# Optimization experiments

Measured on AMD Instinct MI355X. Metric: run time of the kernel, lower is better.

The kernel has to match this reference:

```python
import jax, jax.numpy as jnp
import numpy as np

E = 256
H = 512
LN_EPS = 1e-5
NORM_EPS = 1e-12


def setup_inputs() -> dict:
    key = jax.random.key(0)
    ks = jax.random.split(key, 8)
    B, N, M = 8, 128, 128
    track_features = jax.random.normal(ks[0], (B, N, E), dtype=jnp.float32)
    det_features = jax.random.normal(ks[1], (B, M, E), dtype=jnp.float32)
    # MLP params (torch Linear default init style: uniform, but values irrelevant for correctness harness)
    lim1 = 1.0 / np.sqrt(3 * E)
    W1 = jax.random.uniform(ks[2], (3 * E, H), minval=-lim1, maxval=lim1, dtype=jnp.float32)
    b1 = jax.random.uniform(ks[3], (H,), minval=-lim1, maxval=lim1, dtype=jnp.float32)
    gamma = jnp.ones((H,), dtype=jnp.float32)
    beta = jnp.zeros((H,), dtype=jnp.float32)
    lim2 = 1.0 / np.sqrt(H)
    W2 = jax.random.uniform(ks[4], (H, 1), minval=-lim2, maxval=lim2, dtype=jnp.float32)
    b2 = jax.random.uniform(ks[5], (1,), minval=-lim2, maxval=lim2, dtype=jnp.float32)
    return {"track_features": track_features, "det_features": det_features,
            "W1": W1, "b1": b1, "gamma": gamma, "beta": beta, "W2": W2, "b2": b2}


def _l2_normalize(x):
    # F.normalize(x, dim=-1): x / max(||x||_2, eps)
    n = jnp.sqrt(jnp.sum(x * x, axis=-1, keepdims=True))
    return x / jnp.maximum(n, NORM_EPS)


def reference(track_features, det_features, W1, b1, gamma, beta, W2, b2):
    t = _l2_normalize(track_features)   # (B, N, E)
    d = _l2_normalize(det_features)     # (B, M, E)
    tb = t[:, :, None, :]               # (B, N, 1, E)
    db = d[:, None, :, :]               # (B, 1, M, E)
    B, N, _ = t.shape
    M = d.shape[1]
    diff = jnp.abs(tb - db)                                  # (B, N, M, E)
    pair = jnp.concatenate([jnp.broadcast_to(tb, (B, N, M, E)),
                            jnp.broadcast_to(db, (B, N, M, E)),
                            diff], axis=-1)                  # (B, N, M, 3E)
    h = jnp.einsum('bnme,eh->bnmh', pair, W1) + b1           # (B, N, M, H)
    mu = jnp.mean(h, axis=-1, keepdims=True)
    var = jnp.mean((h - mu) ** 2, axis=-1, keepdims=True)
    h = (h - mu) * jax.lax.rsqrt(var + LN_EPS) * gamma + beta
    h = h * jax.nn.sigmoid(h)                                # SiLU
    out = jnp.einsum('bnmh,ho->bnmo', h, W2)[..., 0] + b2[0]  # (B, N, M)
    return out
```

## Files before the change

kernel.cpp:

```cpp
#include <hip/hip_runtime.h>
#include <hip/hip_bf16.h>
#include <cstdint>

typedef __bf16 bf16x8 __attribute__((ext_vector_type(8)));
typedef __bf16 bf16x2 __attribute__((ext_vector_type(2)));
typedef float f32x4 __attribute__((ext_vector_type(4)));
typedef float f32x2 __attribute__((ext_vector_type(2)));

#define E_DIM 256
#define H_DIM 512

static __device__ __forceinline__ unsigned pkbf(float a, float b) {
    bf16x2 h;
    h[0] = (__bf16)a;
    h[1] = (__bf16)b;
    return __builtin_bit_cast(unsigned, h);
}

__global__ __launch_bounds__(512, 2)
void prep_kernel(const float* __restrict__ track, const float* __restrict__ det,
                 const float* __restrict__ W1, const float* __restrict__ b1,
                 float* __restrict__ P, float* __restrict__ Q,
                 __bf16* __restrict__ W1cc, float* __restrict__ sclT,
                 float* __restrict__ sclD, float* __restrict__ out) {
    __shared__ __align__(16) __bf16 Ash[16 * 256];
    int tid  = threadIdx.x;
    int blk  = blockIdx.x;
    int lane = tid & 63;
    int wave = tid >> 6;
    int lq   = lane >> 4;
    int lc   = lane & 15;
    int l5   = lane & 31;

    int mat  = blk >> 8;
    int rowg = (blk >> 2) & 63;
    int hq   = blk & 3;
    int r0   = rowg * 16;
    int h0   = hq * 128;
    const float* src = mat ? det : track;

    if (tid < 32) {
        int u = blk * 32 + tid;
        int j = u & 3;
        int h = (u >> 2) & 511;
        int c = u >> 11;
        const float* s = W1 + (size_t)(512 + c * 32 + j * 8) * H_DIM + h;
        uint4 v;
        v.x = pkbf(s[0],                 s[(size_t)1 * H_DIM]);
        v.y = pkbf(s[(size_t)2 * H_DIM], s[(size_t)3 * H_DIM]);
        v.z = pkbf(s[(size_t)4 * H_DIM], s[(size_t)5 * H_DIM]);
        v.w = pkbf(s[(size_t)6 * H_DIM], s[(size_t)7 * H_DIM]);
        *(uint4*)(W1cc + ((size_t)(c * 512 + h) * 32 + j * 8)) = v;
    } else if (tid < 96) {
        float4 z = {0.f, 0.f, 0.f, 0.f};
        ((float4*)out)[blk * 64 + (tid - 32)] = z;
    }

    {
        int row = wave * 2 + (lane >> 5);
        const float* gp = src + (size_t)(r0 + row) * E_DIM + l5 * 8;
        float4 x0 = *(const float4*)gp;
        float4 x1 = *(const float4*)(gp + 4);
        float ss = x0.x*x0.x + x0.y*x0.y + x0.z*x0.z + x0.w*x0.w
                 + x1.x*x1.x + x1.y*x1.y + x1.z*x1.z + x1.w*x1.w;
#pragma unroll
        for (int off = 16; off > 0; off >>= 1) ss += __shfl_xor(ss, off);
        float st = 1.0f / fmaxf(sqrtf(ss), 1e-12f);
        if (hq == 0 && l5 == 0) (mat ? sclD : sclT)[r0 + row] = st;
        uint4 v;
        v.x = pkbf(x0.x * st, x0.y * st);
        v.y = pkbf(x0.z * st, x0.w * st);
        v.z = pkbf(x1.x * st, x1.y * st);
        v.w = pkbf(x1.z * st, x1.w * st);
        int cc = l5 >> 2, j = l5 & 3;
        *(uint4*)&Ash[(size_t)(cc * 64 + j * 16 + row) * 8] = v;
    }
    __syncthreads();

    int hB = h0 + wave * 16 + lc;
    const float* wb = W1 + (size_t)(mat * 256) * H_DIM + hB;
    float wf[8];
#pragma unroll
    for (int i = 0; i < 8; ++i)
        wf[i] = wb[(size_t)(lq * 8 + i) * H_DIM];

    f32x4 acc = (f32x4){0.f, 0.f, 0.f, 0.f};

#pragma unroll
    for (int c = 0; c < 8; ++c) {
        uint4 u;
        u.x = pkbf(wf[0], wf[1]);
        u.y = pkbf(wf[2], wf[3]);
        u.z = pkbf(wf[4], wf[5]);
        u.w = pkbf(wf[6], wf[7]);
        bf16x8 cw = __builtin_bit_cast(bf16x8, u);
        if (c < 7) {
            const float* nb = wb + (size_t)((c + 1) * 32 + lq * 8) * H_DIM;
#pragma unroll
            for (int i = 0; i < 8; ++i)
                wf[i] = nb[(size_t)i * H_DIM];
        }
        bf16x8 af = *(const bf16x8*)&Ash[(size_t)(c * 64 + lane) * 8];
        acc = __builtin_amdgcn_mfma_f32_16x16x32_bf16(cw, af, acc, 0, 0, 0);
    }

    float* dst = mat ? Q : P;
    int h = h0 + wave * 16 + lq * 4;
    f32x4 o = acc;
    if (!mat) o += *(const f32x4*)&b1[h];
    *(f32x4*)&dst[(size_t)(r0 + lc) * H_DIM + h] = o;
}

__global__ __launch_bounds__(512, 4)
void main_kernel(const float* __restrict__ track, const float* __restrict__ det,
                 const __bf16* __restrict__ W1cc,
                 const float* __restrict__ P, const float* __restrict__ Q,
                 const float* __restrict__ sclT, const float* __restrict__ sclD,
                 const float* __restrict__ gamma, const float* __restrict__ beta,
                 const float* __restrict__ W2, const float* __restrict__ b2,
                 float* __restrict__ out) {
    __shared__ __align__(16) char SMEM[44032];
    __bf16* Ash  = (__bf16*)SMEM;
    float*  LNr1 = (float*)(SMEM + 32768);
    float*  LNr2 = (float*)(SMEM + 35072);
    float*  AS   = (float*)(SMEM + 37376);
    float*  BS   = (float*)(SMEM + 37632);
    float*  Gs   = (float*)(SMEM + 37888);
    float*  Bs   = (float*)(SMEM + 39936);
    float*  Ws   = (float*)(SMEM + 41984);

    int tid  = threadIdx.x;
    int lane = tid & 63;
    int wave = tid >> 6;
    int lq   = lane >> 4;
    int lc   = lane & 15;

    int i   = blockIdx.x;
    int xcd = i & 7;
    int t8  = (i >> 3) & 31;
    int b   = i >> 8;
    int n0  = ((xcd >> 1) * 4 + (t8 >> 3)) * 8;
    int m0  = ((xcd & 1) * 8 + (t8 & 7)) * 8;
    int gn  = b * 128 + n0;
    int gm  = b * 128 + m0;

    float b2v = b2[0];
    Gs[tid] = gamma[tid];
    Bs[tid] = beta[tid];
    Ws[tid] = W2[tid];

    const uint4* Wg = (const uint4*)W1cc;
    int hb = wave * 64 + lc;
    bf16x8 bwA[4], bwB[4];
#pragma unroll
    for (int ht = 0; ht < 4; ++ht)
        bwA[ht] = __builtin_bit_cast(bf16x8, Wg[(hb + ht * 16) * 4 + lq]);

    int k0 = wave * 32 + lq * 8;
    int ml = lane & 7;
    float sd = sclD[gm + ml];
    const float* dr = det + (size_t)(gm + ml) * E_DIM + k0;
    float4 d0 = *(const float4*)dr;
    float4 d1 = *(const float4*)(dr + 4);
#pragma unroll
    for (int r = 0; r < 4; ++r) {
        int nl = r * 2 + (lc >> 3);
        float st = sclT[gn + nl];
        const float* tr = track + (size_t)(gn + nl) * E_DIM + k0;
        float4 t0 = *(const float4*)tr;
        float4 t1 = *(const float4*)(tr + 4);
        uint4 v;
        v.x = pkbf(fabsf(t0.x * st - d0.x * sd), fabsf(t0.y * st - d0.y * sd));
        v.y = pkbf(fabsf(t0.z * st - d0.z * sd), fabsf(t0.w * st - d0.w * sd));
        v.z = pkbf(fabsf(t1.x * st - d1.x * sd), fabsf(t1.y * st - d1.y * sd));
        v.w = pkbf(fabsf(t1.z * st - d1.z * sd), fabsf(t1.w * st - d1.w * sd));
        *(uint4*)&Ash[(size_t)(r * 512 + wave * 64 + lane) * 8] = v;
    }

    const float* Pb = P + (size_t)gn * H_DIM;
    const float* Qb = Q + (size_t)gm * H_DIM;
    f32x4 acc[4][4];
    {
        f32x4 qv[4];
#pragma unroll
        for (int ht = 0; ht < 4; ++ht)
            qv[ht] = *(const f32x4*)&Qb[(size_t)ml * H_DIM + wave * 64 + ht * 16 + lq * 4];
#pragma unroll
        for (int pt = 0; pt < 4; ++pt) {
            int n = pt * 2 + (lc >> 3);
#pragma unroll
            for (int ht = 0; ht < 4; ++ht) {
                f32x4 pv = *(const f32x4*)&Pb[(size_t)n * H_DIM + wave * 64 + ht * 16 + lq * 4];
                acc[pt][ht] = pv + qv[ht];
            }
        }
    }
    __syncthreads();

#pragma unroll 2
    for (int c = 0; c < 8; ++c) {
        bf16x8* cur = (c & 1) ? bwB : bwA;
        bf16x8* nxt = (c & 1) ? bwA : bwB;
        int c1 = (c + 1) & 7;
#pragma unroll
        for (int ht = 0; ht < 4; ++ht)
            nxt[ht] = __builtin_bit_cast(bf16x8, Wg[c1 * 2048 + (hb + ht * 16) * 4 + lq]);
        __builtin_amdgcn_s_setprio(1);
#pragma unroll
        for (int pt = 0; pt < 4; ++pt) {
            bf16x8 af = *(const bf16x8*)&Ash[(size_t)((pt * 8 + c) * 64 + lane) * 8];
#pragma unroll
            for (int ht = 0; ht < 4; ++ht)
                acc[pt][ht] = __builtin_amdgcn_mfma_f32_16x16x32_bf16(cur[ht], af, acc[pt][ht], 0, 0, 0);
        }
        __builtin_amdgcn_s_setprio(0);
    }

#pragma unroll
    for (int pt = 0; pt < 4; ++pt) {
        f32x2 s1v = (f32x2){0.f, 0.f}, s2v = (f32x2){0.f, 0.f};
#pragma unroll
        for (int ht = 0; ht < 4; ++ht) {
#pragma unroll
            for (int hf = 0; hf < 2; ++hf) {
                f32x2 v = (f32x2){acc[pt][ht][hf * 2], acc[pt][ht][hf * 2 + 1]};
                s1v += v;
                s2v += v * v;
            }
        }
        float s1 = s1v[0] + s1v[1];
        float s2 = s2v[0] + s2v[1];
        s1 += __shfl_xor(s1, 16); s2 += __shfl_xor(s2, 16);
        s1 += __shfl_xor(s1, 32); s2 += __shfl_xor(s2, 32);
        if (lq == 0) {
            LNr1[(pt * 16 + lc) * 9 + wave] = s1;
            LNr2[(pt * 16 + lc) * 9 + wave] = s2;
        }
    }
    __syncthreads();
    {
        int p = tid >> 3, w = tid & 7;
        float s1 = LNr1[p * 9 + w];
        float s2 = LNr2[p * 9 + w];
        s1 += __shfl_xor(s1, 1); s2 += __shfl_xor(s2, 1);
        s1 += __shfl_xor(s1, 2); s2 += __shfl_xor(s2, 2);
        s1 += __shfl_xor(s1, 4); s2 += __shfl_xor(s2, 4);
        if (w == 0) {
            float mu  = s1 * (1.0f / 512.0f);
            float var = s2 * (1.0f / 512.0f) - mu * mu;
            float rs  = rsqrtf(var + 1e-5f);
            AS[p] = rs;
            BS[p] = -mu * rs;
        }
    }
    __syncthreads();

    float as[4], bs[4];
#pragma unroll
    for (int pt = 0; pt < 4; ++pt) { as[pt] = AS[pt * 16 + lc]; bs[pt] = BS[pt * 16 + lc]; }
    f32x2 cav[4];
#pragma unroll
    for (int pt = 0; pt < 4; ++pt) cav[pt] = (f32x2){0.f, 0.f};
#pragma unroll
    for (int ht = 0; ht < 4; ++ht) {
        int h = wave * 64 + ht * 16 + lq * 4;
        f32x4 g  = *(const f32x4*)&Gs[h];
        f32x4 bb = *(const f32x4*)&Bs[h];
        f32x4 w  = *(const f32x4*)&Ws[h];
#pragma unroll
        for (int pt = 0; pt < 4; ++pt) {
            f32x2 a2  = (f32x2){as[pt], as[pt]};
            f32x2 b2p = (f32x2){bs[pt], bs[pt]};
#pragma unroll
            for (int hf = 0; hf < 2; ++hf) {
                f32x2 v  = (f32x2){acc[pt][ht][hf * 2], acc[pt][ht][hf * 2 + 1]};
                f32x2 gg = (f32x2){g[hf * 2],  g[hf * 2 + 1]};
                f32x2 bv = (f32x2){bb[hf * 2], bb[hf * 2 + 1]};
                f32x2 wv = (f32x2){w[hf * 2],  w[hf * 2 + 1]};
                f32x2 x  = (v * a2 + b2p) * gg + bv;
                f32x2 xw = x * wv;
                f32x2 e, sg;
                e[0]  = __expf(-x[0]);
                e[1]  = __expf(-x[1]);
                sg[0] = __builtin_amdgcn_rcpf(1.0f + e[0]);
                sg[1] = __builtin_amdgcn_rcpf(1.0f + e[1]);
                cav[pt] += xw * sg;
            }
        }
    }
#pragma unroll
    for (int pt = 0; pt < 4; ++pt) {
        float cg = cav[pt][0] + cav[pt][1];
        cg += __shfl_xor(cg, 16);
        cg += __shfl_xor(cg, 32);
        if (lq == 0) {
            if (wave == 0) cg += b2v;
            int n = pt * 2 + (lc >> 3);
            int m = lc & 7;
            atomicAdd(&out[(size_t)(gn + n) * 128 + m0 + m], cg);
        }
    }
}

extern "C" void kernel_launch(void* const* d_in, const int* in_sizes, int n_in,
                              void* d_out, int out_size, void* d_ws, size_t ws_size,
                              hipStream_t stream) {
    const float* track = (const float*)d_in[0];
    const float* det   = (const float*)d_in[1];
    const float* W1    = (const float*)d_in[2];
    const float* b1    = (const float*)d_in[3];
    const float* gamma = (const float*)d_in[4];
    const float* beta  = (const float*)d_in[5];
    const float* W2    = (const float*)d_in[6];
    const float* b2    = (const float*)d_in[7];
    float* out = (float*)d_out;

    char* ws = (char*)d_ws;
    float*  Pp   = (float*)(ws);
    float*  Qp   = (float*)(ws + (2u << 20));
    __bf16* W1cc = (__bf16*)(ws + (4u << 20));
    float*  sclT = (float*)(ws + (4u << 20) + (256u << 10));
    float*  sclD = (float*)(ws + (4u << 20) + (264u << 10));

    prep_kernel<<<512, 512, 0, stream>>>(track, det, W1, b1, Pp, Qp, W1cc, sclT, sclD, out);
    main_kernel<<<2048, 512, 0, stream>>>(track, det, W1cc, Pp, Qp, sclT, sclD,
                                          gamma, beta, W2, b2, out);
}
```

Baseline: 142.2 us.

## Process two detection tiles per block with overlapped next-tile staging

Each main_kernel block now handles two consecutive 8-row detection tiles for the same 8 track rows, halving the grid to 1024 blocks. The second tile's pair-difference staging into shared memory is issued between the LayerNorm reduction barriers, and its P+Q accumulator init is issued after the first tile's atomics. The goal is to amortize per-block setup (gamma/beta/W2 staging, first W1 fragment loads) and overlap global loads with epilogue work. The cost is half as many blocks to fill the device and a longer serial chain within each block.

```diff
diff --git a/kernel.cpp b/kernel.cpp
--- a/kernel.cpp
+++ b/kernel.cpp
@@ -110,6 +110,47 @@
     if (!mat) o += *(const f32x4*)&b1[h];
     *(f32x4*)&dst[(size_t)(r0 + lc) * H_DIM + h] = o;
 }
+
+#define A_STAGE(GM)                                                                     \
+    {                                                                                   \
+        int k0 = wave * 32 + lq * 8;                                                    \
+        float sd = sclD[(GM) + ml];                                                     \
+        const float* drp = det + (size_t)((GM) + ml) * E_DIM + k0;                      \
+        float4 d0 = *(const float4*)drp;                                                \
+        float4 d1 = *(const float4*)(drp + 4);                                          \
+        _Pragma("unroll")                                                               \
+        for (int r = 0; r < 4; ++r) {                                                   \
+            int nl = r * 2 + (lc >> 3);                                                 \
+            float st = sclT[gn + nl];                                                   \
+            const float* trp = track + (size_t)(gn + nl) * E_DIM + k0;                  \
+            float4 t0 = *(const float4*)trp;                                            \
+            float4 t1 = *(const float4*)(trp + 4);                                      \
+            uint4 vv;                                                                   \
+            vv.x = pkbf(fabsf(t0.x * st - d0.x * sd), fabsf(t0.y * st - d0.y * sd));    \
+            vv.y = pkbf(fabsf(t0.z * st - d0.z * sd), fabsf(t0.w * st - d0.w * sd));    \
+            vv.z = pkbf(fabsf(t1.x * st - d1.x * sd), fabsf(t1.y * st - d1.y * sd));    \
+            vv.w = pkbf(fabsf(t1.z * st - d1.z * sd), fabsf(t1.w * st - d1.w * sd));    \
+            *(uint4*)&Ash[(size_t)(r * 512 + wave * 64 + lane) * 8] = vv;               \
+        }                                                                               \
+    }
+
+#define C_INIT(GM)                                                                      \
+    {                                                                                   \
+        const float* Qb = Q + (size_t)(GM) * H_DIM;                                     \
+        f32x4 qv[4];                                                                    \
+        _Pragma("unroll")                                                               \
+        for (int ht = 0; ht < 4; ++ht)                                                  \
+            qv[ht] = *(const f32x4*)&Qb[(size_t)ml * H_DIM + wave * 64 + ht * 16 + lq * 4]; \
+        _Pragma("unroll")                                                               \
+        for (int pt = 0; pt < 4; ++pt) {                                                \
+            int n = pt * 2 + (lc >> 3);                                                 \
+            _Pragma("unroll")                                                           \
+            for (int ht = 0; ht < 4; ++ht) {                                            \
+                f32x4 pv = *(const f32x4*)&Pb[(size_t)n * H_DIM + wave * 64 + ht * 16 + lq * 4]; \
+                acc[pt][ht] = pv + qv[ht];                                              \
+            }                                                                           \
+        }                                                                               \
+    }
 
 __global__ __launch_bounds__(512, 4)
 void main_kernel(const float* __restrict__ track, const float* __restrict__ det,
@@ -134,15 +175,16 @@
     int wave = tid >> 6;
     int lq   = lane >> 4;
     int lc   = lane & 15;
+    int ml   = lane & 7;
 
     int i   = blockIdx.x;
     int xcd = i & 7;
-    int t8  = (i >> 3) & 31;
-    int b   = i >> 8;
-    int n0  = ((xcd >> 1) * 4 + (t8 >> 3)) * 8;
-    int m0  = ((xcd & 1) * 8 + (t8 & 7)) * 8;
+    int t4  = (i >> 3) & 15;
+    int b   = i >> 7;
+    int n0  = ((xcd >> 1) * 4 + (t4 >> 2)) * 8;
+    int mp0 = ((xcd & 1) * 4 + (t4 & 3)) * 16;
     int gn  = b * 128 + n0;
-    int gm  = b * 128 + m0;
+    int gm0 = b * 128 + mp0;
 
     float b2v = b2[0];
     Gs[tid] = gamma[tid];
@@ -156,148 +198,123 @@
     for (int ht = 0; ht < 4; ++ht)
         bwA[ht] = __builtin_bit_cast(bf16x8, Wg[(hb + ht * 16) * 4 + lq]);
 
-    int k0 = wave * 32 + lq * 8;
-    int ml = lane & 7;
-    float sd = sclD[gm + ml];
-    const float* dr = det + (size_t)(gm + ml) * E_DIM + k0;
-    float4 d0 = *(const float4*)dr;
-    float4 d1 = *(const float4*)(dr + 4);
-#pragma unroll
-    for (int r = 0; r < 4; ++r) {
-        int nl = r * 2 + (lc >> 3);
-        float st = sclT[gn + nl];
-        const float* tr = track + (size_t)(gn + nl) * E_DIM + k0;
-        float4 t0 = *(const float4*)tr;
-        float4 t1 = *(const float4*)(tr + 4);
-        uint4 v;
-        v.x = pkbf(fabsf(t0.x * st - d0.x * sd), fabsf(t0.y * st - d0.y * sd));
-        v.y = pkbf(fabsf(t0.z * st - d0.z * sd), fabsf(t0.w * st - d0.w * sd));
-        v.z = pkbf(fabsf(t1.x * st - d1.x * sd), fabsf(t1.y * st - d1.y * sd));
-        v.w = pkbf(fabsf(t1.z * st - d1.z * sd), fabsf(t1.w * st - d1.w * sd));
-        *(uint4*)&Ash[(size_t)(r * 512 + wave * 64 + lane) * 8] = v;
-    }
-
     const float* Pb = P + (size_t)gn * H_DIM;
-    const float* Qb = Q + (size_t)gm * H_DIM;
     f32x4 acc[4][4];
-    {
-        f32x4 qv[4];
-#pragma unroll
-        for (int ht = 0; ht < 4; ++ht)
-            qv[ht] = *(const f32x4*)&Qb[(size_t)ml * H_DIM + wave * 64 + ht * 16 + lq * 4];
+
+    A_STAGE(gm0)
+    C_INIT(gm0)
+    __syncthreads();
+
+#pragma unroll 1
+    for (int j = 0; j < 2; ++j) {
+#pragma unroll 2
+        for (int c = 0; c < 8; ++c) {
+            bf16x8* cur = (c & 1) ? bwB : bwA;
+            bf16x8* nxt = (c & 1) ? bwA : bwB;
+            int c1 = (c + 1) & 7;
+#pragma unroll
+            for (int ht = 0; ht < 4; ++ht)
+                nxt[ht] = __builtin_bit_cast(bf16x8, Wg[c1 * 2048 + (hb + ht * 16) * 4 + lq]);
+            __builtin_amdgcn_s_setprio(1);
+#pragma unroll
+            for (int pt = 0; pt < 4; ++pt) {
+                bf16x8 af = *(const bf16x8*)&Ash[(size_t)((pt * 8 + c) * 64 + lane) * 8];
+#pragma unroll
+                for (int ht = 0; ht < 4; ++ht)
+                    acc[pt][ht] = __builtin_amdgcn_mfma_f32_16x16x32_bf16(cur[ht], af, acc[pt][ht], 0, 0, 0);
+            }
+            __builtin_amdgcn_s_setprio(0);
+        }
+
 #pragma unroll
         for (int pt = 0; pt < 4; ++pt) {
-            int n = pt * 2 + (lc >> 3);
+            f32x2 s1v = (f32x2){0.f, 0.f}, s2v = (f32x2){0.f, 0.f};
 #pragma unroll
             for (int ht = 0; ht < 4; ++ht) {
-                f32x4 pv = *(const f32x4*)&Pb[(size_t)n * H_DIM + wave * 64 + ht * 16 + lq * 4];
-                acc[pt][ht] = pv + qv[ht];
-            }
-        }
-    }
-    __syncthreads();
-
-#pragma unroll 2
-    for (int c = 0; c < 8; ++c) {
-        bf16x8* cur = (c & 1) ? bwB : bwA;
-        bf16x8* nxt = (c & 1) ? bwA : bwB;
-        int c1 = (c + 1) & 7;
-#pragma unroll
-        for (int ht = 0; ht < 4; ++ht)
-            nxt[ht] = __builtin_bit_cast(bf16x8, Wg[c1 * 2048 + (hb + ht * 16) * 4 + lq]);
-        __builtin_amdgcn_s_setprio(1);
+#pragma unroll
+                for (int hf = 0; hf < 2; ++hf) {
+                    f32x2 v = (f32x2){acc[pt][ht][hf * 2], acc[pt][ht][hf * 2 + 1]};
+                    s1v += v;
+                    s2v += v * v;
+                }
+            }
+            float s1 = s1v[0] + s1v[1];
+            float s2 = s2v[0] + s2v[1];
+            s1 += __shfl_xor(s1, 16); s2 += __shfl_xor(s2, 16);
+            s1 += __shfl_xor(s1, 32); s2 += __shfl_xor(s2, 32);
+            if (lq == 0) {
+                LNr1[(pt * 16 + lc) * 9 + wave] = s1;
+                LNr2[(pt * 16 + lc) * 9 + wave] = s2;
+            }
+        }
+        __syncthreads();
+        {
+            int p = tid >> 3, w = tid & 7;
+            float s1 = LNr1[p * 9 + w];
+            float s2 = LNr2[p * 9 + w];
+            s1 += __shfl_xor(s1, 1); s2 += __shfl_xor(s2, 1);
+            s1 += __shfl_xor(s1, 2); s2 += __shfl_xor(s2, 2);
+            s1 += __shfl_xor(s1, 4); s2 += __shfl_xor(s2, 4);
+            if (w == 0) {
+                float mu  = s1 * (1.0f / 512.0f);
+                float var = s2 * (1.0f / 512.0f) - mu * mu;
+                float rs  = rsqrtf(var + 1e-5f);
+                AS[p] = rs;
+                BS[p] = -mu * rs;
+            }
+        }
+        if (j == 0) {
+            A_STAGE(gm0 + 8)
+        }
+        __syncthreads();
+
+        float as[4], bs[4];
+#pragma unroll
+        for (int pt = 0; pt < 4; ++pt) { as[pt] = AS[pt * 16 + lc]; bs[pt] = BS[pt * 16 + lc]; }
+        f32x2 cav[4];
+#pragma unroll
+        for (int pt = 0; pt < 4; ++pt) cav[pt] = (f32x2){0.f, 0.f};
+#pragma unroll
+        for (int ht = 0; ht < 4; ++ht) {
+            int h = wave * 64 + ht * 16 + lq * 4;
+            f32x4 g  = *(const f32x4*)&Gs[h];
+            f32x4 bb = *(const f32x4*)&Bs[h];
+            f32x4 w  = *(const f32x4*)&Ws[h];
+#pragma unroll
+            for (int pt = 0; pt < 4; ++pt) {
+                f32x2 a2  = (f32x2){as[pt], as[pt]};
+                f32x2 b2p = (f32x2){bs[pt], bs[pt]};
+#pragma unroll
+                for (int hf = 0; hf < 2; ++hf) {
+                    f32x2 v  = (f32x2){acc[pt][ht][hf * 2], acc[pt][ht][hf * 2 + 1]};
+                    f32x2 gg = (f32x2){g[hf * 2],  g[hf * 2 + 1]};
+                    f32x2 bv = (f32x2){bb[hf * 2], bb[hf * 2 + 1]};
+                    f32x2 wv = (f32x2){w[hf * 2],  w[hf * 2 + 1]};
+                    f32x2 x  = (v * a2 + b2p) * gg + bv;
+                    f32x2 xw = x * wv;
+                    f32x2 e, sg;
+                    e[0]  = __expf(-x[0]);
+                    e[1]  = __expf(-x[1]);
+                    sg[0] = __builtin_amdgcn_rcpf(1.0f + e[0]);
+                    sg[1] = __builtin_amdgcn_rcpf(1.0f + e[1]);
+                    cav[pt] += xw * sg;
+                }
+            }
+        }
 #pragma unroll
         for (int pt = 0; pt < 4; ++pt) {
-            bf16x8 af = *(const bf16x8*)&Ash[(size_t)((pt * 8 + c) * 64 + lane) * 8];
-#pragma unroll
-            for (int ht = 0; ht < 4; ++ht)
-                acc[pt][ht] = __builtin_amdgcn_mfma_f32_16x16x32_bf16(cur[ht], af, acc[pt][ht], 0, 0, 0);
-        }
-        __builtin_amdgcn_s_setprio(0);
-    }
-
-#pragma unroll
-    for (int pt = 0; pt < 4; ++pt) {
-        f32x2 s1v = (f32x2){0.f, 0.f}, s2v = (f32x2){0.f, 0.f};
-#pragma unroll
-        for (int ht = 0; ht < 4; ++ht) {
-#pragma unroll
-            for (int hf = 0; hf < 2; ++hf) {
-                f32x2 v = (f32x2){acc[pt][ht][hf * 2], acc[pt][ht][hf * 2 + 1]};
-                s1v += v;
-                s2v += v * v;
-            }
-        }
-        float s1 = s1v[0] + s1v[1];
-        float s2 = s2v[0] + s2v[1];
-        s1 += __shfl_xor(s1, 16); s2 += __shfl_xor(s2, 16);
-        s1 += __shfl_xor(s1, 32); s2 += __shfl_xor(s2, 32);
-        if (lq == 0) {
-            LNr1[(pt * 16 + lc) * 9 + wave] = s1;
-            LNr2[(pt * 16 + lc) * 9 + wave] = s2;
-        }
-    }
-    __syncthreads();
-    {
-        int p = tid >> 3, w = tid & 7;
-        float s1 = LNr1[p * 9 + w];
-        float s2 = LNr2[p * 9 + w];
-        s1 += __shfl_xor(s1, 1); s2 += __shfl_xor(s2, 1);
-        s1 += __shfl_xor(s1, 2); s2 += __shfl_xor(s2, 2);
-        s1 += __shfl_xor(s1, 4); s2 += __shfl_xor(s2, 4);
-        if (w == 0) {
-            float mu  = s1 * (1.0f / 512.0f);
-            float var = s2 * (1.0f / 512.0f) - mu * mu;
-            float rs  = rsqrtf(var + 1e-5f);
-            AS[p] = rs;
-            BS[p] = -mu * rs;
-        }
-    }
-    __syncthreads();
-
-    float as[4], bs[4];
-#pragma unroll
-    for (int pt = 0; pt < 4; ++pt) { as[pt] = AS[pt * 16 + lc]; bs[pt] = BS[pt * 16 + lc]; }
-    f32x2 cav[4];
-#pragma unroll
-    for (int pt = 0; pt < 4; ++pt) cav[pt] = (f32x2){0.f, 0.f};
-#pragma unroll
-    for (int ht = 0; ht < 4; ++ht) {
-        int h = wave * 64 + ht * 16 + lq * 4;
-        f32x4 g  = *(const f32x4*)&Gs[h];
-        f32x4 bb = *(const f32x4*)&Bs[h];
-        f32x4 w  = *(const f32x4*)&Ws[h];
-#pragma unroll
-        for (int pt = 0; pt < 4; ++pt) {
-            f32x2 a2  = (f32x2){as[pt], as[pt]};
-            f32x2 b2p = (f32x2){bs[pt], bs[pt]};
-#pragma unroll
-            for (int hf = 0; hf < 2; ++hf) {
-                f32x2 v  = (f32x2){acc[pt][ht][hf * 2], acc[pt][ht][hf * 2 + 1]};
-                f32x2 gg = (f32x2){g[hf * 2],  g[hf * 2 + 1]};
-                f32x2 bv = (f32x2){bb[hf * 2], bb[hf * 2 + 1]};
-                f32x2 wv = (f32x2){w[hf * 2],  w[hf * 2 + 1]};
-                f32x2 x  = (v * a2 + b2p) * gg + bv;
-                f32x2 xw = x * wv;
-                f32x2 e, sg;
-                e[0]  = __expf(-x[0]);
-                e[1]  = __expf(-x[1]);
-                sg[0] = __builtin_amdgcn_rcpf(1.0f + e[0]);
-                sg[1] = __builtin_amdgcn_rcpf(1.0f + e[1]);
-                cav[pt] += xw * sg;
-            }
-        }
-    }
-#pragma unroll
-    for (int pt = 0; pt < 4; ++pt) {
-        float cg = cav[pt][0] + cav[pt][1];
-        cg += __shfl_xor(cg, 16);
-        cg += __shfl_xor(cg, 32);
-        if (lq == 0) {
-            if (wave == 0) cg += b2v;
-            int n = pt * 2 + (lc >> 3);
-            int m = lc & 7;
-            atomicAdd(&out[(size_t)(gn + n) * 128 + m0 + m], cg);
+            float cg = cav[pt][0] + cav[pt][1];
+            cg += __shfl_xor(cg, 16);
+            cg += __shfl_xor(cg, 32);
+            if (lq == 0) {
+                if (wave == 0) cg += b2v;
+                int n = pt * 2 + (lc >> 3);
+                int m = lc & 7;
+                atomicAdd(&out[(size_t)(gn + n) * 128 + mp0 + j * 8 + m], cg);
+            }
+        }
+        if (j == 0) {
+            C_INIT(gm0 + 8)
         }
     }
 }
@@ -323,6 +340,6 @@
     float*  sclD = (float*)(ws + (4u << 20) + (264u << 10));
 
     prep_kernel<<<512, 512, 0, stream>>>(track, det, W1, b1, Pp, Qp, W1cc, sclT, sclD, out);
-    main_kernel<<<2048, 512, 0, stream>>>(track, det, W1cc, Pp, Qp, sclT, sclD,
+    main_kernel<<<1024, 512, 0, stream>>>(track, det, W1cc, Pp, Qp, sclT, sclD,
                                           gamma, beta, W2, b2, out);
 }
```

After: 186.5 us. 31.1% more time.
